# Kernel optimization log

Hardware: AMD Instinct MI355X
Metric: run time of the kernel (lower is better)

## Reference

```python
import jax, jax.numpy as jnp
import numpy as np

NUM_GRAPHS = 128

def _gcn_conv(x, W, b, src, dst, deg_inv_sqrt, n_nodes):
    # PyG GCNConv: h = X W; out[dst] += d^-1/2[src] * d^-1/2[dst] * h[src]; out += b
    h = x @ W
    norm = deg_inv_sqrt[src] * deg_inv_sqrt[dst]  # [E]
    msg = h[src] * norm[:, None]                  # [E, C]
    out = jax.ops.segment_sum(msg, dst, num_segments=n_nodes)
    return out + b


def setup_inputs() -> dict:
    key = jax.random.key(0)
    k1, k2, k3, k4, k5 = jax.random.split(key, 5)
    n_nodes, n_edges, c_in, c_hid = 50000, 800000, 256, 256
    x = jax.random.normal(k1, (n_nodes, c_in), dtype=jnp.float32)
    edge_index = jax.random.randint(k2, (2, n_edges), 0, n_nodes, dtype=jnp.int64)
    batch = jnp.sort(jax.random.randint(k3, (n_nodes,), 0, NUM_GRAPHS, dtype=jnp.int64))
    s1 = 1.0 / np.sqrt(c_in)
    s2 = 1.0 / np.sqrt(c_hid)
    W1 = jax.random.uniform(k4, (c_in, c_hid), jnp.float32, -s1, s1)
    b1 = jnp.zeros((c_hid,), jnp.float32)
    W2 = jax.random.uniform(k5, (c_hid, c_hid), jnp.float32, -s2, s2)
    b2 = jnp.zeros((c_hid,), jnp.float32)
    return {"x": x, "edge_index": edge_index, "batch": batch,
            "W1": W1, "b1": b1, "W2": W2, "b2": b2}


def reference(x, edge_index, batch, W1, b1, W2, b2):
    n_nodes = x.shape[0]
    # add self-loops (GCNConv default add_self_loops=True)
    loops = jnp.arange(n_nodes, dtype=edge_index.dtype)
    src = jnp.concatenate([edge_index[0], loops])
    dst = jnp.concatenate([edge_index[1], loops])
    deg = jax.ops.segment_sum(jnp.ones_like(dst, dtype=x.dtype), dst, num_segments=n_nodes)
    deg_inv_sqrt = jnp.where(deg > 0, jax.lax.rsqrt(deg), 0.0)

    h = jax.nn.relu(_gcn_conv(x, W1, b1, src, dst, deg_inv_sqrt, n_nodes))
    # dropout p=0.2 is identity in eval mode
    h = jax.nn.relu(_gcn_conv(h, W2, b2, src, dst, deg_inv_sqrt, n_nodes))

    # global mean pool over graph ids
    sums = jax.ops.segment_sum(h, batch, num_segments=NUM_GRAPHS)
    cnts = jax.ops.segment_sum(jnp.ones((n_nodes,), h.dtype), batch, num_segments=NUM_GRAPHS)
    return sums / jnp.maximum(cnts, 1.0)[:, None]
```

## Files before the change

### kernel.cpp

```cpp
#include <hip/hip_runtime.h>

#define NCH 256
#define NS  16

typedef short short8 __attribute__((ext_vector_type(8)));
typedef float f32x4  __attribute__((ext_vector_type(4)));

__device__ __forceinline__ float b2f(unsigned short u) {
    union { unsigned int i; float f; } x; x.i = ((unsigned int)u) << 16; return x.f;
}
__device__ __forceinline__ unsigned short f2b(float f) {
    unsigned int u = __float_as_uint(f);
    unsigned int r = (u + 0x7FFFu + ((u >> 16) & 1u)) >> 16;
    return (unsigned short)r;
}

#define GLOAD_LDS16(gptr, lptr) \
    __builtin_amdgcn_global_load_lds((const __attribute__((address_space(1))) void*)(gptr), \
                                     (__attribute__((address_space(3))) void*)(lptr), 16, 0, 0)

__global__ __launch_bounds__(256) void k_hist(const int* __restrict__ dst, int E,
                                              int* __restrict__ deg) {
    int e = blockIdx.x * 256 + threadIdx.x;
    if (e < E) atomicAdd(&deg[dst[e]], 1);
}

__global__ __launch_bounds__(256) void k_scan_blk(const int* __restrict__ deg,
                                                  int* __restrict__ part,
                                                  int* __restrict__ bsum, int N) {
    __shared__ int sm[256];
    int t = threadIdx.x;
    int base = blockIdx.x * 1024 + t * 4;
    int v[4]; int s = 0;
#pragma unroll
    for (int j = 0; j < 4; ++j) {
        int i = base + j;
        int d = (i < N) ? deg[i] : 0;
        v[j] = d; s += d;
    }
    sm[t] = s; __syncthreads();
#pragma unroll
    for (int off = 1; off < 256; off <<= 1) {
        int u = (t >= off) ? sm[t - off] : 0;
        __syncthreads();
        sm[t] += u;
        __syncthreads();
    }
    int excl = sm[t] - s;
#pragma unroll
    for (int j = 0; j < 4; ++j) {
        int i = base + j;
        if (i < N) part[i] = excl;
        excl += v[j];
    }
    if (t == 255) bsum[blockIdx.x] = sm[255];
}

__global__ void k_scan_top(int* __restrict__ bsum, int nb, int* __restrict__ rowptr_end) {
    int t = threadIdx.x;
    int orig = (t < nb) ? bsum[t] : 0;
    int v = orig;
#pragma unroll
    for (int off = 1; off < 64; off <<= 1) {
        int u = __shfl_up(v, off, 64);
        if (t >= off) v += u;
    }
    if (t < nb) bsum[t] = v - orig;
    if (t == 63) *rowptr_end = v;
}

__global__ __launch_bounds__(256) void k_finalize(const int* __restrict__ deg,
                                                  int* __restrict__ row_ptr,
                                                  const int* __restrict__ boff,
                                                  int* __restrict__ cursor,
                                                  float* __restrict__ dinv, int N) {
    int i = blockIdx.x * 256 + threadIdx.x;
    if (i < N) {
        int rp = row_ptr[i] + boff[i >> 10];
        row_ptr[i] = rp;
        cursor[i]  = rp;
        dinv[i] = rsqrtf((float)(deg[i] + 1));
    }
}

__global__ __launch_bounds__(256) void k_scatter_sh(const int* __restrict__ src,
                                                    const int* __restrict__ dst, int E,
                                                    int* __restrict__ cursor,
                                                    const float* __restrict__ dinv,
                                                    int2* __restrict__ cw,
                                                    unsigned shmul) {
    const int shard  = blockIdx.x & 7;
    const int nchunk = gridDim.x >> 3;
    const int chunk  = blockIdx.x >> 3;
    const int per = (E + nchunk - 1) / nchunk;
    const int e0 = chunk * per;
    const int e1 = min(e0 + per, E);
    for (int e = e0 + threadIdx.x; e < e1; e += 256) {
        int d = dst[e];
        int s = (int)__umulhi((unsigned)d, shmul);
        if (s == shard) {
            int sv = src[e];
            int pos = atomicAdd(&cursor[d], 1);
            cw[pos] = make_int2(sv, __float_as_int(dinv[sv]));
        }
    }
}

__global__ __launch_bounds__(256) void k_cast8(const float* __restrict__ in,
                                               unsigned short* __restrict__ out, int n8) {
    int i = blockIdx.x * 256 + threadIdx.x;
    if (i < n8) {
        const float4* p = (const float4*)(in + (size_t)i * 8);
        float4 a = p[0], b = p[1];
        unsigned short us[8];
        us[0] = f2b(a.x); us[1] = f2b(a.y); us[2] = f2b(a.z); us[3] = f2b(a.w);
        us[4] = f2b(b.x); us[5] = f2b(b.y); us[6] = f2b(b.z); us[7] = f2b(b.w);
        *(int4*)(out + (size_t)i * 8) = *(const int4*)us;
    }
}

__global__ __launch_bounds__(256) void k_castT(const float* __restrict__ W1,
                                               const float* __restrict__ W2,
                                               unsigned short* __restrict__ Wt1,
                                               unsigned short* __restrict__ Wt2) {
    int k = blockIdx.x, n = threadIdx.x;
    const float* W = blockIdx.y ? W2 : W1;
    unsigned short* Wt = blockIdx.y ? Wt2 : Wt1;
    Wt[(size_t)n * 256 + k] = f2b(W[(size_t)k * 256 + n]);
}

__global__ __launch_bounds__(512, 4) void k_gemm_lds(const unsigned short* __restrict__ A,
                                                     const unsigned short* __restrict__ Bt,
                                                     unsigned short* __restrict__ C,
                                                     int M, int tiles) {
    __shared__ unsigned short As[32 * 256];

    const int tid  = threadIdx.x;
    const int w    = tid >> 6;
    const int lane = tid & 63;
    const int lr   = lane & 15;
    const int ku   = lane >> 4;

    short8 bfr[2][8];
    {
        const unsigned short* pb = Bt + (size_t)(w * 32 + lr) * NCH + ku * 8;
#pragma unroll
        for (int nf = 0; nf < 2; ++nf)
#pragma unroll
            for (int ks = 0; ks < 8; ++ks)
                bfr[nf][ks] = *(const short8*)(pb + nf * 16 * NCH + ks * 32);
    }

    const int gu0 = w * 128 + lane;
    for (int t = blockIdx.x; t < tiles; t += gridDim.x) {
        __syncthreads();
#pragma unroll
        for (int j = 0; j < 2; ++j) {
            int gu = gu0 + j * 64;
            int r  = gu >> 5;
            int u  = gu & 31;
            int grow = t * 32 + r; if (grow >= M) grow = M - 1;
            const unsigned short* gp = A + (size_t)grow * NCH + ((u ^ (r & 7)) << 3);
            GLOAD_LDS16(gp, As + (size_t)(w * 128 + j * 64) * 8);
        }
        __syncthreads();

        f32x4 acc[2][2];
#pragma unroll
        for (int rf = 0; rf < 2; ++rf)
#pragma unroll
            for (int nf = 0; nf < 2; ++nf) acc[rf][nf] = (f32x4){0.f, 0.f, 0.f, 0.f};

#pragma unroll
        for (int ks = 0; ks < 8; ++ks) {
#pragma unroll
            for (int rf = 0; rf < 2; ++rf) {
                int row = rf * 16 + lr;
                int uu  = (ks * 4 + ku) ^ (row & 7);
                short8 af = *(const short8*)&As[row * 256 + uu * 8];
                acc[rf][0] = __builtin_amdgcn_mfma_f32_16x16x32_bf16(bfr[0][ks], af,
                                                                     acc[rf][0], 0, 0, 0);
                acc[rf][1] = __builtin_amdgcn_mfma_f32_16x16x32_bf16(bfr[1][ks], af,
                                                                     acc[rf][1], 0, 0, 0);
            }
        }

#pragma unroll
        for (int rf = 0; rf < 2; ++rf) {
            int row = t * 32 + rf * 16 + lr;
            if (row < M) {
                unsigned short* pc = C + (size_t)row * NCH + w * 32 + ku * 4;
#pragma unroll
                for (int nf = 0; nf < 2; ++nf) {
                    unsigned short us[4];
                    us[0] = f2b(acc[rf][nf][0]); us[1] = f2b(acc[rf][nf][1]);
                    us[2] = f2b(acc[rf][nf][2]); us[3] = f2b(acc[rf][nf][3]);
                    *(int2*)(pc + nf * 16) = *(const int2*)us;
                }
            }
        }
    }
}

__global__ __launch_bounds__(256) void k_agg_w(const unsigned short* __restrict__ h,
                                               const float* __restrict__ dinv,
                                               const int* __restrict__ row_ptr,
                                               const int2* __restrict__ cw,
                                               const float* __restrict__ bias,
                                               unsigned short* __restrict__ out, int M) {
    int v = blockIdx.x * 4 + (threadIdx.x >> 6);
    if (v >= M) return;
    const int lane = threadIdx.x & 63;
    const int half = lane >> 5;
    const int cb   = (lane & 31) << 3;

    float acc[8] = {};
    float dv = dinv[v];

    short8 rs = {};
    if (half == 0) rs = *(const short8*)&h[(size_t)v * NCH + cb];

    int beg = row_ptr[v], end = row_ptr[v + 1];
    int i0 = beg + half * 2;

    short8 r0 = {}, r1 = {};
    float  w0 = 0.f, w1 = 0.f;
    bool b0 = i0 < end, b1 = i0 + 1 < end;
    if (b0) {
        int2 e = cw[i0];
        r0 = *(const short8*)&h[(size_t)e.x * NCH + cb];
        w0 = __int_as_float(e.y);
    }
    if (b1) {
        int2 e = cw[i0 + 1];
        r1 = *(const short8*)&h[(size_t)e.x * NCH + cb];
        w1 = __int_as_float(e.y);
    }

    while (b0) {
        int in = i0 + 4;
        bool n0 = in < end, n1 = in + 1 < end;
        short8 s0 = {}, s1 = {};
        float  x0 = 0.f, x1 = 0.f;
        if (n0) {
            int2 e = cw[in];
            s0 = *(const short8*)&h[(size_t)e.x * NCH + cb];
            x0 = __int_as_float(e.y);
        }
        if (n1) {
            int2 e = cw[in + 1];
            s1 = *(const short8*)&h[(size_t)e.x * NCH + cb];
            x1 = __int_as_float(e.y);
        }
#pragma unroll
        for (int i = 0; i < 8; ++i) acc[i] += w0 * b2f((unsigned short)r0[i]);
#pragma unroll
        for (int i = 0; i < 8; ++i) acc[i] += w1 * b2f((unsigned short)r1[i]);
        r0 = s0; r1 = s1; w0 = x0; w1 = x1; b0 = n0; b1 = n1; i0 = in;
    }

    if (half == 0) {
#pragma unroll
        for (int i = 0; i < 8; ++i) acc[i] += dv * b2f((unsigned short)rs[i]);
    }

#pragma unroll
    for (int i = 0; i < 8; ++i) acc[i] += __shfl_xor(acc[i], 32, 64);

    if (half == 0) {
        f32x4 bl = *(const f32x4*)&bias[cb];
        f32x4 bh = *(const f32x4*)&bias[cb + 4];
        unsigned short us[8];
#pragma unroll
        for (int i = 0; i < 8; ++i) {
            float b = (i < 4) ? bl[i] : bh[i - 4];
            us[i] = f2b(fmaxf(dv * acc[i] + b, 0.0f));
        }
        *(int4*)&out[(size_t)v * NCH + cb] = *(const int4*)us;
    }
}

__device__ __forceinline__ int lower_bound_i(const int* a, int n, int key) {
    int lo = 0, hi = n;
    while (lo < hi) {
        int mid = (lo + hi) >> 1;
        if (a[mid] < key) lo = mid + 1; else hi = mid;
    }
    return lo;
}

__global__ __launch_bounds__(64) void k_pool_a(const unsigned short* __restrict__ a,
                                               const int* __restrict__ batch,
                                               float* __restrict__ partial, int N) {
    int g = blockIdx.x, s = blockIdx.y;
    const int lane = threadIdx.x;
    const int half = lane >> 5;
    const int cb   = (lane & 31) << 3;

    int lo = lower_bound_i(batch, N, g);
    int hi = lower_bound_i(batch, N, g + 1);
    int cnt = hi - lo;
    int len = (cnt + NS - 1) / NS;
    int rlo = lo + s * len;
    int rhi = min(rlo + len, hi);

    float acc[8] = {};
    for (int r = rlo + half; r < rhi; r += 2) {
        short8 hv = *(const short8*)&a[(size_t)r * NCH + cb];
#pragma unroll
        for (int i = 0; i < 8; ++i) acc[i] += b2f((unsigned short)hv[i]);
    }
#pragma unroll
    for (int i = 0; i < 8; ++i) acc[i] += __shfl_xor(acc[i], 32, 64);

    if (half == 0) {
        float* p = partial + ((size_t)g * NS + s) * NCH + cb;
        *(f32x4*)p       = (f32x4){acc[0], acc[1], acc[2], acc[3]};
        *(f32x4*)(p + 4) = (f32x4){acc[4], acc[5], acc[6], acc[7]};
    }
}

__global__ __launch_bounds__(256) void k_pool_b(const float* __restrict__ partial,
                                                const int* __restrict__ batch,
                                                float* __restrict__ out, int N) {
    int g = blockIdx.x, ch = threadIdx.x;
    int lo = lower_bound_i(batch, N, g);
    int hi = lower_bound_i(batch, N, g + 1);
    float s = 0.0f;
#pragma unroll
    for (int k = 0; k < NS; ++k)
        s += partial[((size_t)g * NS + k) * NCH + ch];
    out[(size_t)g * NCH + ch] = s / (float)max(hi - lo, 1);
}

extern "C" void kernel_launch(void* const* d_in, const int* in_sizes, int n_in,
                              void* d_out, int out_size, void* d_ws, size_t ws_size,
                              hipStream_t stream) {
    const float* x     = (const float*)d_in[0];
    const int*   ei    = (const int*)d_in[1];
    const int*   batch = (const int*)d_in[2];
    const float* W1    = (const float*)d_in[3];
    const float* b1    = (const float*)d_in[4];
    const float* W2    = (const float*)d_in[5];
    const float* b2    = (const float*)d_in[6];
    float* out = (float*)d_out;

    const int M = in_sizes[0] / NCH;
    const int E = in_sizes[1] / 2;
    const int* src = ei;
    const int* dst = ei + E;

    char* w = (char*)d_ws;
    auto alloc = [&](size_t bytes) -> void* {
        void* p = (void*)w;
        w += (bytes + 255) & ~(size_t)255;
        return p;
    };
    int*   deg     = (int*)alloc((size_t)M * 4);
    float* dinv    = (float*)alloc((size_t)M * 4);
    int*   row_ptr = (int*)alloc((size_t)(M + 1) * 4);
    int*   cursor  = (int*)alloc((size_t)M * 4);
    int*   bsum    = (int*)alloc(64 * 4);
    int2*  cw      = (int2*)alloc((size_t)E * 8);
    unsigned short* xb   = (unsigned short*)alloc((size_t)M * NCH * 2);
    unsigned short* bufP = (unsigned short*)alloc((size_t)M * NCH * 2);
    unsigned short* bufQ = (unsigned short*)alloc((size_t)M * NCH * 2);
    unsigned short* Wt1  = (unsigned short*)alloc((size_t)NCH * NCH * 2);
    unsigned short* Wt2  = (unsigned short*)alloc((size_t)NCH * NCH * 2);
    float* partial = (float*)alloc((size_t)128 * NS * NCH * 4);

    const int nb = (M + 1023) / 1024;
    const unsigned shmul = (unsigned)(((8ull << 32) + M - 1) / (unsigned long long)M);
    const int tiles = (M + 31) / 32;

    k_cast8<<<(M * NCH / 8 + 255) / 256, 256, 0, stream>>>(x, xb, M * NCH / 8);
    k_castT<<<dim3(256, 2), 256, 0, stream>>>(W1, W2, Wt1, Wt2);

    hipMemsetAsync(deg, 0, (size_t)M * 4, stream);
    k_hist<<<(E + 255) / 256, 256, 0, stream>>>(dst, E, deg);
    k_scan_blk<<<nb, 256, 0, stream>>>(deg, row_ptr, bsum, M);
    k_scan_top<<<1, 64, 0, stream>>>(bsum, nb, row_ptr + M);
    k_finalize<<<(M + 255) / 256, 256, 0, stream>>>(deg, row_ptr, bsum, cursor, dinv, M);
    k_scatter_sh<<<2048, 256, 0, stream>>>(src, dst, E, cursor, dinv, cw, shmul);

    const int ggrid = 512;
    const int agrid = (M + 3) / 4;

    k_gemm_lds<<<ggrid, 512, 0, stream>>>(xb, Wt1, bufP, M, tiles);
    k_agg_w<<<agrid, 256, 0, stream>>>(bufP, dinv, row_ptr, cw, b1, bufQ, M);
    k_gemm_lds<<<ggrid, 512, 0, stream>>>(bufQ, Wt2, bufP, M, tiles);
    k_agg_w<<<agrid, 256, 0, stream>>>(bufP, dinv, row_ptr, cw, b2, bufQ, M);
    k_pool_a<<<dim3(128, NS), 64, 0, stream>>>(bufQ, batch, partial, M);
    k_pool_b<<<128, 256, 0, stream>>>(partial, batch, out, M);
}
```

Baseline: 287.7 us.

## Fuse histogram with cast, double-buffer GEMM LDS, split aggregation launches

Merges the degree histogram and the x-to-bf16 cast into one launch, using block-index ranges so the memset is the only dependency. The GEMM now double-buffers its LDS A tile so the next tile's global-to-LDS load is issued before the MFMAs on the current one, aiming to hide load latency. It doubles LDS use, which can lower occupancy. Each aggregation pass is also split into two launches over node halves, which adds launch overhead without any evident concurrency gain.

Measured after the change: 299.4 us. 4.1% more time.

```diff
diff --git a/kernel.cpp b/kernel.cpp
--- a/kernel.cpp
+++ b/kernel.cpp
@@ -19,10 +19,25 @@
     __builtin_amdgcn_global_load_lds((const __attribute__((address_space(1))) void*)(gptr), \
                                      (__attribute__((address_space(3))) void*)(lptr), 16, 0, 0)
 
-__global__ __launch_bounds__(256) void k_hist(const int* __restrict__ dst, int E,
-                                              int* __restrict__ deg) {
-    int e = blockIdx.x * 256 + threadIdx.x;
-    if (e < E) atomicAdd(&deg[dst[e]], 1);
+__global__ __launch_bounds__(256) void k_pre(const float* __restrict__ x,
+                                             unsigned short* __restrict__ xb, int n8,
+                                             const int* __restrict__ dst, int E,
+                                             int* __restrict__ deg, int nh) {
+    int b = blockIdx.x;
+    if (b < nh) {
+        int e = b * 256 + threadIdx.x;
+        if (e < E) atomicAdd(&deg[dst[e]], 1);
+    } else {
+        int i = (b - nh) * 256 + threadIdx.x;
+        if (i < n8) {
+            const float4* p = (const float4*)(x + (size_t)i * 8);
+            float4 a = p[0], c = p[1];
+            unsigned short us[8];
+            us[0] = f2b(a.x); us[1] = f2b(a.y); us[2] = f2b(a.z); us[3] = f2b(a.w);
+            us[4] = f2b(c.x); us[5] = f2b(c.y); us[6] = f2b(c.z); us[7] = f2b(c.w);
+            *(int4*)(xb + (size_t)i * 8) = *(const int4*)us;
+        }
+    }
 }
 
 __global__ __launch_bounds__(256) void k_scan_blk(const int* __restrict__ deg,
@@ -106,19 +121,6 @@
     }
 }
 
-__global__ __launch_bounds__(256) void k_cast8(const float* __restrict__ in,
-                                               unsigned short* __restrict__ out, int n8) {
-    int i = blockIdx.x * 256 + threadIdx.x;
-    if (i < n8) {
-        const float4* p = (const float4*)(in + (size_t)i * 8);
-        float4 a = p[0], b = p[1];
-        unsigned short us[8];
-        us[0] = f2b(a.x); us[1] = f2b(a.y); us[2] = f2b(a.z); us[3] = f2b(a.w);
-        us[4] = f2b(b.x); us[5] = f2b(b.y); us[6] = f2b(b.z); us[7] = f2b(b.w);
-        *(int4*)(out + (size_t)i * 8) = *(const int4*)us;
-    }
-}
-
 __global__ __launch_bounds__(256) void k_castT(const float* __restrict__ W1,
                                                const float* __restrict__ W2,
                                                unsigned short* __restrict__ Wt1,
@@ -133,7 +135,7 @@
                                                      const unsigned short* __restrict__ Bt,
                                                      unsigned short* __restrict__ C,
                                                      int M, int tiles) {
-    __shared__ unsigned short As[32 * 256];
+    __shared__ unsigned short As[2][32 * 256];
 
     const int tid  = threadIdx.x;
     const int w    = tid >> 6;
@@ -152,18 +154,28 @@
     }
 
     const int gu0 = w * 128 + lane;
-    for (int t = blockIdx.x; t < tiles; t += gridDim.x) {
-        __syncthreads();
-#pragma unroll
-        for (int j = 0; j < 2; ++j) {
-            int gu = gu0 + j * 64;
-            int r  = gu >> 5;
-            int u  = gu & 31;
-            int grow = t * 32 + r; if (grow >= M) grow = M - 1;
-            const unsigned short* gp = A + (size_t)grow * NCH + ((u ^ (r & 7)) << 3);
-            GLOAD_LDS16(gp, As + (size_t)(w * 128 + j * 64) * 8);
-        }
-        __syncthreads();
+
+#define STAGE(tt, buf) do {                                                   \
+        _Pragma("unroll")                                                     \
+        for (int j = 0; j < 2; ++j) {                                         \
+            int gu = gu0 + j * 64;                                            \
+            int r  = gu >> 5;                                                 \
+            int u  = gu & 31;                                                 \
+            int grow = (tt) * 32 + r; if (grow >= M) grow = M - 1;            \
+            const unsigned short* gp = A + (size_t)grow * NCH +               \
+                                       ((u ^ (r & 7)) << 3);                  \
+            GLOAD_LDS16(gp, (buf) + (size_t)(w * 128 + j * 64) * 8);          \
+        }                                                                     \
+    } while (0)
+
+    int t = blockIdx.x;
+    int cur = 0;
+    if (t < tiles) STAGE(t, As[0]);
+    __syncthreads();
+
+    for (; t < tiles; t += gridDim.x) {
+        int tn = t + gridDim.x;
+        if (tn < tiles) STAGE(tn, As[cur ^ 1]);
 
         f32x4 acc[2][2];
 #pragma unroll
@@ -177,7 +189,7 @@
             for (int rf = 0; rf < 2; ++rf) {
                 int row = rf * 16 + lr;
                 int uu  = (ks * 4 + ku) ^ (row & 7);
-                short8 af = *(const short8*)&As[row * 256 + uu * 8];
+                short8 af = *(const short8*)&As[cur][row * 256 + uu * 8];
                 acc[rf][0] = __builtin_amdgcn_mfma_f32_16x16x32_bf16(bfr[0][ks], af,
                                                                      acc[rf][0], 0, 0, 0);
                 acc[rf][1] = __builtin_amdgcn_mfma_f32_16x16x32_bf16(bfr[1][ks], af,
@@ -199,7 +211,10 @@
                 }
             }
         }
-    }
+        __syncthreads();
+        cur ^= 1;
+    }
+#undef STAGE
 }
 
 __global__ __launch_bounds__(256) void k_agg_w(const unsigned short* __restrict__ h,
@@ -207,9 +222,10 @@
                                                const int* __restrict__ row_ptr,
                                                const int2* __restrict__ cw,
                                                const float* __restrict__ bias,
-                                               unsigned short* __restrict__ out, int M) {
-    int v = blockIdx.x * 4 + (threadIdx.x >> 6);
-    if (v >= M) return;
+                                               unsigned short* __restrict__ out,
+                                               int v0, int vend) {
+    int v = v0 + blockIdx.x * 4 + (threadIdx.x >> 6);
+    if (v >= vend) return;
     const int lane = threadIdx.x & 63;
     const int half = lane >> 5;
     const int cb   = (lane & 31) << 3;
@@ -372,24 +388,28 @@
     const int nb = (M + 1023) / 1024;
     const unsigned shmul = (unsigned)(((8ull << 32) + M - 1) / (unsigned long long)M);
     const int tiles = (M + 31) / 32;
-
-    k_cast8<<<(M * NCH / 8 + 255) / 256, 256, 0, stream>>>(x, xb, M * NCH / 8);
+    const int nh = (E + 255) / 256;
+    const int n8 = M * NCH / 8;
+    const int nc = (n8 + 255) / 256;
+
+    hipMemsetAsync(deg, 0, (size_t)M * 4, stream);
+    k_pre<<<nh + nc, 256, 0, stream>>>(x, xb, n8, dst, E, deg, nh);
     k_castT<<<dim3(256, 2), 256, 0, stream>>>(W1, W2, Wt1, Wt2);
-
-    hipMemsetAsync(deg, 0, (size_t)M * 4, stream);
-    k_hist<<<(E + 255) / 256, 256, 0, stream>>>(dst, E, deg);
     k_scan_blk<<<nb, 256, 0, stream>>>(deg, row_ptr, bsum, M);
     k_scan_top<<<1, 64, 0, stream>>>(bsum, nb, row_ptr + M);
     k_finalize<<<(M + 255) / 256, 256, 0, stream>>>(deg, row_ptr, bsum, cursor, dinv, M);
     k_scatter_sh<<<2048, 256, 0, stream>>>(src, dst, E, cursor, dinv, cw, shmul);
 
     const int ggrid = 512;
-    const int agrid = (M + 3) / 4;
+    const int Mh = M / 2;
+    const int agrid = (Mh + 3) / 4;
 
     k_gemm_lds<<<ggrid, 512, 0, stream>>>(xb, Wt1, bufP, M, tiles);
-    k_agg_w<<<agrid, 256, 0, stream>>>(bufP, dinv, row_ptr, cw, b1, bufQ, M);
+    k_agg_w<<<agrid, 256, 0, stream>>>(bufP, dinv, row_ptr, cw, b1, bufQ, 0, Mh);
+    k_agg_w<<<(M - Mh + 3) / 4, 256, 0, stream>>>(bufP, dinv, row_ptr, cw, b1, bufQ, Mh, M);
     k_gemm_lds<<<ggrid, 512, 0, stream>>>(bufQ, Wt2, bufP, M, tiles);
-    k_agg_w<<<agrid, 256, 0, stream>>>(bufP, dinv, row_ptr, cw, b2, bufQ, M);
+    k_agg_w<<<agrid, 256, 0, stream>>>(bufP, dinv, row_ptr, cw, b2, bufQ, 0, Mh);
+    k_agg_w<<<(M - Mh + 3) / 4, 256, 0, stream>>>(bufP, dinv, row_ptr, cw, b2, bufQ, Mh, M);
     k_pool_a<<<dim3(128, NS), 64, 0, stream>>>(bufQ, batch, partial, M);
     k_pool_b<<<128, 256, 0, stream>>>(partial, batch, out, M);
 }
```
